# Kernel optimization log

Measured on AMD Instinct MI355X. Metric: run time of the kernel, lower is better.

Reference implementation:

```python
import jax, jax.numpy as jnp
import numpy as np


def setup_inputs() -> dict:
    key = jax.random.key(0)
    k1, = jax.random.split(key, 1)
    x = jax.random.normal(k1, (8, 256, 128, 128), dtype=jnp.float32)
    alpha = jnp.ones((1,), dtype=jnp.float32)
    return {"x": x, "alpha": alpha}


def reference(x, alpha):
    B, C, H, W = x.shape
    v = x.reshape(B, C, H * W)                 # [B, C, HW] (query=key=value)
    energy = jnp.einsum('bcs,bds->bcd', v, v)  # [B, C, C]
    # max-softmax: softmax(max(energy) - energy) along last dim
    energy_new = jnp.max(energy, axis=-1, keepdims=True) - energy
    w = jax.nn.softmax(energy_new, axis=-1)    # [B, C, C]
    y = jnp.einsum('bcd,bds->bcs', w, v)       # [B, C, HW]
    y = y.reshape(B, C, H, W)
    return alpha * y + x
```

## Files before the change

### kernel.cpp

```cpp
#include <hip/hip_runtime.h>
#include <math.h>

static constexpr int Bn = 8;
static constexpr int Cn = 256;
static constexpr int Sn = 16384;

typedef __bf16 bf16x4 __attribute__((ext_vector_type(4)));
typedef __bf16 bf16x8 __attribute__((ext_vector_type(8)));
typedef float  f32x4  __attribute__((ext_vector_type(4)));

__device__ __forceinline__ void split_store(__bf16* __restrict__ Hi, __bf16* __restrict__ Lo,
                                            int row, int kq, float4 v) {
  __bf16 h0 = (__bf16)v.x, h1 = (__bf16)v.y, h2 = (__bf16)v.z, h3 = (__bf16)v.w;
  int off = row * 32 + (((kq >> 1) ^ (row & 3)) << 3) + ((kq & 1) << 2);
  *(bf16x4*)&Hi[off] = (bf16x4){h0, h1, h2, h3};
  *(bf16x4*)&Lo[off] = (bf16x4){(__bf16)(v.x - (float)h0), (__bf16)(v.y - (float)h1),
                                (__bf16)(v.z - (float)h2), (__bf16)(v.w - (float)h3)};
}

__device__ __forceinline__ bf16x8 frag_ld(const __bf16* __restrict__ P, int row, int quad) {
  return *(const bf16x8*)&P[row * 32 + ((quad ^ (row & 3)) << 3)];
}

static constexpr int TILE   = 128;
static constexpr int KSPLIT = 16;
static constexpr int KSLICE = Sn / KSPLIT;
static constexpr int KB     = 32;

__global__ __launch_bounds__(256, 2) void gram_kernel(const float* __restrict__ x,
                                                      float* __restrict__ energy) {
  const int b    = blockIdx.z;
  const int tsel = blockIdx.y;
  const int kk   = blockIdx.x;
  const int ti   = (tsel == 1) ? 1 : 0;
  const int tj   = (tsel == 0) ? 0 : 1;
  const bool diag = (tsel < 2);

  const float* vb    = x + (size_t)b * Cn * Sn;
  const float* Abase = vb + (size_t)(ti * TILE) * Sn + kk * KSLICE;
  const float* Bbase = vb + (size_t)(tj * TILE) * Sn + kk * KSLICE;

  __shared__ __align__(16) __bf16 Ah[TILE * 32];
  __shared__ __align__(16) __bf16 Al[TILE * 32];
  __shared__ __align__(16) __bf16 Bh[TILE * 32];
  __shared__ __align__(16) __bf16 Bl[TILE * 32];

  const int t    = threadIdx.x;
  const int lane = t & 63;
  const int wv   = t >> 6;
  const int wr   = wv >> 1;
  const int wc   = wv & 1;
  const int ln   = lane & 15;
  const int quad = lane >> 4;

  const int srow = t >> 3;
  const int skq  = t & 7;

  float4 areg[4], breg[4];

#pragma unroll
  for (int it = 0; it < 4; it++)
    areg[it] = *(const float4*)(Abase + (size_t)(srow + it * 32) * Sn + skq * 4);
  if (!diag) {
#pragma unroll
    for (int it = 0; it < 4; it++)
      breg[it] = *(const float4*)(Bbase + (size_t)(srow + it * 32) * Sn + skq * 4);
  }

  f32x4 acc[4][4];
#pragma unroll
  for (int i = 0; i < 4; i++)
#pragma unroll
    for (int j = 0; j < 4; j++) acc[i][j] = (f32x4){0.f, 0.f, 0.f, 0.f};

  for (int kc = 0; kc < KSLICE; kc += KB) {
#pragma unroll
    for (int it = 0; it < 4; it++) split_store(Ah, Al, srow + it * 32, skq, areg[it]);
    if (!diag) {
#pragma unroll
      for (int it = 0; it < 4; it++) split_store(Bh, Bl, srow + it * 32, skq, breg[it]);
    }
    __syncthreads();

    const __bf16* PH = diag ? Ah : Bh;
    const __bf16* PL = diag ? Al : Bl;

    bf16x8 fah[4], fal[4];
#pragma unroll
    for (int i = 0; i < 4; i++) {
      int ar = wr * 64 + i * 16 + ln;
      fah[i] = frag_ld(Ah, ar, quad);
      fal[i] = frag_ld(Al, ar, quad);
    }

    if (kc + KB < KSLICE) {
#pragma unroll
      for (int it = 0; it < 4; it++)
        areg[it] = *(const float4*)(Abase + (size_t)(srow + it * 32) * Sn + (kc + KB) + skq * 4);
      if (!diag) {
#pragma unroll
        for (int it = 0; it < 4; it++)
          breg[it] = *(const float4*)(Bbase + (size_t)(srow + it * 32) * Sn + (kc + KB) + skq * 4);
      }
    }

#pragma unroll
    for (int j = 0; j < 4; j++) {
      int br = wc * 64 + j * 16 + ln;
      bf16x8 fbh = frag_ld(PH, br, quad);
      bf16x8 fbl = frag_ld(PL, br, quad);
#pragma unroll
      for (int i = 0; i < 4; i++) {
        acc[i][j] = __builtin_amdgcn_mfma_f32_16x16x32_bf16(fah[i], fbh, acc[i][j], 0, 0, 0);
        acc[i][j] = __builtin_amdgcn_mfma_f32_16x16x32_bf16(fah[i], fbl, acc[i][j], 0, 0, 0);
        acc[i][j] = __builtin_amdgcn_mfma_f32_16x16x32_bf16(fal[i], fbh, acc[i][j], 0, 0, 0);
      }
    }
    __syncthreads();
  }

  float* E = energy + (size_t)b * Cn * Cn;
#pragma unroll
  for (int i = 0; i < 4; i++)
#pragma unroll
    for (int j = 0; j < 4; j++) {
      int c0 = ti * TILE + wr * 64 + i * 16 + quad * 4;
      int d  = tj * TILE + wc * 64 + j * 16 + ln;
#pragma unroll
      for (int r = 0; r < 4; r++) {
        float v = acc[i][j][r];
        atomicAdd(&E[(size_t)(c0 + r) * Cn + d], v);
        if (tsel == 2) atomicAdd(&E[(size_t)d * Cn + (c0 + r)], v);
      }
    }
}

__global__ __launch_bounds__(256) void softmax_kernel(float* __restrict__ energy) {
  const int wv   = threadIdx.x >> 6;
  const int lane = threadIdx.x & 63;
  const int row  = blockIdx.x * 4 + wv;

  float4 e = *(const float4*)&energy[(size_t)row * Cn + lane * 4];
  float m = fminf(fminf(e.x, e.y), fminf(e.z, e.w));
#pragma unroll
  for (int off = 32; off > 0; off >>= 1) m = fminf(m, __shfl_xor(m, off));

  float4 p;
  p.x = expf(m - e.x); p.y = expf(m - e.y);
  p.z = expf(m - e.z); p.w = expf(m - e.w);
  float s = p.x + p.y + p.z + p.w;
#pragma unroll
  for (int off = 32; off > 0; off >>= 1) s += __shfl_xor(s, off);

  float inv = 1.f / s;
  p.x *= inv; p.y *= inv; p.z *= inv; p.w *= inv;
  *(float4*)&energy[(size_t)row * Cn + lane * 4] = p;
}

__global__ __launch_bounds__(256, 2) void ygemm_mfma_kernel(const float* __restrict__ w,
                                                            const float* __restrict__ x,
                                                            const float* __restrict__ alpha,
                                                            float* __restrict__ out) {
  const int b  = blockIdx.z;
  const int m0 = blockIdx.y * 128;
  const int s0 = blockIdx.x * 128;

  const float* Wb = w + ((size_t)b * Cn + m0) * Cn;
  const float* Vb = x + (size_t)b * Cn * Sn;

  __shared__ __align__(16) __bf16 Ah[128 * 32];
  __shared__ __align__(16) __bf16 Al[128 * 32];
  __shared__ __align__(16) __bf16 Bh[128 * 32];
  __shared__ __align__(16) __bf16 Bl[128 * 32];

  const int t    = threadIdx.x;
  const int lane = t & 63;
  const int wv   = t >> 6;
  const int wr   = wv >> 1;
  const int wc   = wv & 1;
  const int ln   = lane & 15;
  const int quad = lane >> 4;

  const int srow = t >> 3;
  const int skq  = t & 7;

  float4 areg[4];
  float  breg[16];

#pragma unroll
  for (int it = 0; it < 4; it++)
    areg[it] = *(const float4*)(Wb + (size_t)(srow + it * 32) * Cn + skq * 4);
#pragma unroll
  for (int it = 0; it < 4; it++) {
    const float* col = Vb + (size_t)(skq * 4) * Sn + s0 + srow + it * 32;
    breg[it * 4 + 0] = col[0];
    breg[it * 4 + 1] = col[(size_t)Sn];
    breg[it * 4 + 2] = col[(size_t)2 * Sn];
    breg[it * 4 + 3] = col[(size_t)3 * Sn];
  }

  f32x4 acc[4][4];
#pragma unroll
  for (int i = 0; i < 4; i++)
#pragma unroll
    for (int j = 0; j < 4; j++) acc[i][j] = (f32x4){0.f, 0.f, 0.f, 0.f};

  for (int kc = 0; kc < Cn; kc += KB) {
#pragma unroll
    for (int it = 0; it < 4; it++) split_store(Ah, Al, srow + it * 32, skq, areg[it]);
#pragma unroll
    for (int it = 0; it < 4; it++) {
      float4 bv = make_float4(breg[it * 4 + 0], breg[it * 4 + 1],
                              breg[it * 4 + 2], breg[it * 4 + 3]);
      split_store(Bh, Bl, srow + it * 32, skq, bv);
    }
    __syncthreads();

    bf16x8 fah[4], fal[4];
#pragma unroll
    for (int i = 0; i < 4; i++) {
      int ar = wr * 64 + i * 16 + ln;
      fah[i] = frag_ld(Ah, ar, quad);
      fal[i] = frag_ld(Al, ar, quad);
    }

    if (kc + KB < Cn) {
#pragma unroll
      for (int it = 0; it < 4; it++)
        areg[it] = *(const float4*)(Wb + (size_t)(srow + it * 32) * Cn + (kc + KB) + skq * 4);
#pragma unroll
      for (int it = 0; it < 4; it++) {
        const float* col = Vb + (size_t)((kc + KB) + skq * 4) * Sn + s0 + srow + it * 32;
        breg[it * 4 + 0] = col[0];
        breg[it * 4 + 1] = col[(size_t)Sn];
        breg[it * 4 + 2] = col[(size_t)2 * Sn];
        breg[it * 4 + 3] = col[(size_t)3 * Sn];
      }
    }

#pragma unroll
    for (int j = 0; j < 4; j++) {
      int br = wc * 64 + j * 16 + ln;
      bf16x8 fbh = frag_ld(Bh, br, quad);
      bf16x8 fbl = frag_ld(Bl, br, quad);
#pragma unroll
      for (int i = 0; i < 4; i++) {
        acc[i][j] = __builtin_amdgcn_mfma_f32_16x16x32_bf16(fah[i], fbh, acc[i][j], 0, 0, 0);
        acc[i][j] = __builtin_amdgcn_mfma_f32_16x16x32_bf16(fah[i], fbl, acc[i][j], 0, 0, 0);
        acc[i][j] = __builtin_amdgcn_mfma_f32_16x16x32_bf16(fal[i], fbh, acc[i][j], 0, 0, 0);
      }
    }
    __syncthreads();
  }

  const float al = alpha[0];
#pragma unroll
  for (int i = 0; i < 4; i++)
#pragma unroll
    for (int j = 0; j < 4; j++) {
      int c = m0 + wr * 64 + i * 16 + quad * 4;
      int s = s0 + wc * 64 + j * 16 + ln;
      const float* xr = x   + ((size_t)b * Cn + c) * Sn + s;
      float*       op = out + ((size_t)b * Cn + c) * Sn + s;
#pragma unroll
      for (int r = 0; r < 4; r++)
        op[(size_t)r * Sn] = al * acc[i][j][r] + xr[(size_t)r * Sn];
    }
}

extern "C" void kernel_launch(void* const* d_in, const int* in_sizes, int n_in,
                              void* d_out, int out_size, void* d_ws, size_t ws_size,
                              hipStream_t stream) {
  const float* x     = (const float*)d_in[0];
  const float* alpha = (const float*)d_in[1];
  float*       out   = (float*)d_out;
  float*       energy = (float*)d_ws;

  const size_t energy_bytes = (size_t)Bn * Cn * Cn * sizeof(float);
  hipMemsetAsync(energy, 0, energy_bytes, stream);

  dim3 g1(KSPLIT, 3, Bn);
  gram_kernel<<<g1, 256, 0, stream>>>(x, energy);

  softmax_kernel<<<(Bn * Cn) / 4, 256, 0, stream>>>(energy);

  dim3 g3(Sn / 128, Cn / 128, Bn);
  ygemm_mfma_kernel<<<g3, 256, 0, stream>>>(energy, x, alpha, out);
}
```

Before: 350.7 us.

## Fuse memset, Gram, softmax and output GEMM into one persistent kernel

Replaces the memset plus three kernel launches with a single persistent kernel whose grid is sized to occupancy and capped at 512 blocks. The stages (zeroing energy, split-K Gram with atomics, row softmax, output GEMM with residual) are separated by software grid barriers built on global atomic counters. The Gram split is also changed: diagonal tiles use 32 K-slices and the off-diagonal tile uses 64. This aims to remove launch gaps and inter-kernel tails, at the cost of grid-barrier spinning, fewer blocks available to hide latency in the memory-bound GEMM, and a deadlock risk if not all blocks are co-resident.

Measured after the change: 543.8 us. 1.55x slower.

```diff
diff --git a/kernel.cpp b/kernel.cpp
--- a/kernel.cpp
+++ b/kernel.cpp
@@ -8,6 +8,9 @@
 typedef __bf16 bf16x4 __attribute__((ext_vector_type(4)));
 typedef __bf16 bf16x8 __attribute__((ext_vector_type(8)));
 typedef float  f32x4  __attribute__((ext_vector_type(4)));
+
+static constexpr int TILE = 128;
+static constexpr int KB   = 32;
 
 __device__ __forceinline__ void split_store(__bf16* __restrict__ Hi, __bf16* __restrict__ Lo,
                                             int row, int kq, float4 v) {
@@ -22,10 +25,263 @@
   return *(const bf16x8*)&P[row * 32 + ((quad ^ (row & 3)) << 3)];
 }
 
-static constexpr int TILE   = 128;
+__device__ unsigned g_cnt[4] = {0, 0, 0, 0};
+__device__ unsigned g_gen[4] = {0, 0, 0, 0};
+
+__device__ __forceinline__ void grid_barrier(int slot) {
+  __syncthreads();
+  if (threadIdx.x == 0) {
+    __threadfence();
+    unsigned my = __hip_atomic_load(&g_gen[slot], __ATOMIC_RELAXED, __HIP_MEMORY_SCOPE_AGENT);
+    unsigned n  = gridDim.x;
+    unsigned a  = __hip_atomic_fetch_add(&g_cnt[slot], 1u, __ATOMIC_ACQ_REL,
+                                         __HIP_MEMORY_SCOPE_AGENT) + 1u;
+    if (a == n) {
+      __hip_atomic_store(&g_cnt[slot], 0u, __ATOMIC_RELAXED, __HIP_MEMORY_SCOPE_AGENT);
+      __hip_atomic_fetch_add(&g_gen[slot], 1u, __ATOMIC_RELEASE, __HIP_MEMORY_SCOPE_AGENT);
+    } else {
+      while (__hip_atomic_load(&g_gen[slot], __ATOMIC_RELAXED, __HIP_MEMORY_SCOPE_AGENT) == my)
+        __builtin_amdgcn_s_sleep(2);
+    }
+    __threadfence();
+  }
+  __syncthreads();
+}
+
+__global__ __launch_bounds__(256, 2) void fused_kernel(const float* __restrict__ x,
+                                                       const float* __restrict__ alpha,
+                                                       float* __restrict__ out,
+                                                       float* __restrict__ energy) {
+  __shared__ __align__(16) __bf16 Ah[TILE * 32];
+  __shared__ __align__(16) __bf16 Al[TILE * 32];
+  __shared__ __align__(16) __bf16 Bh[TILE * 32];
+  __shared__ __align__(16) __bf16 Bl[TILE * 32];
+
+  const int t    = threadIdx.x;
+  const int lane = t & 63;
+  const int wv   = t >> 6;
+  const int wr   = wv >> 1;
+  const int wc   = wv & 1;
+  const int ln   = lane & 15;
+  const int quad = lane >> 4;
+  const int srow = t >> 3;
+  const int skq  = t & 7;
+
+  {
+    const int total = (Bn * Cn * Cn) / 4;
+    for (int i = blockIdx.x * 256 + t; i < total; i += gridDim.x * 256)
+      *(float4*)&energy[(size_t)i * 4] = (float4){0.f, 0.f, 0.f, 0.f};
+  }
+  grid_barrier(0);
+
+  for (unsigned job = blockIdx.x; job < 1024; job += gridDim.x) {
+    int b, ti, tj, kk, ksl;
+    bool diag;
+    if (job < 512) {
+      b = job >> 6; int r = job & 63;
+      diag = true; ti = tj = (r >> 5); kk = r & 31; ksl = 512;
+    } else {
+      unsigned j2 = job - 512;
+      b = j2 >> 6; kk = j2 & 63;
+      diag = false; ti = 0; tj = 1; ksl = 256;
+    }
+
+    const float* vb    = x + (size_t)b * Cn * Sn;
+    const float* Abase = vb + (size_t)(ti * TILE) * Sn + (size_t)kk * ksl;
+    const float* Bbase = vb + (size_t)(tj * TILE) * Sn + (size_t)kk * ksl;
+
+    float4 areg[4], breg[4];
+#pragma unroll
+    for (int it = 0; it < 4; it++)
+      areg[it] = *(const float4*)(Abase + (size_t)(srow + it * 32) * Sn + skq * 4);
+    if (!diag) {
+#pragma unroll
+      for (int it = 0; it < 4; it++)
+        breg[it] = *(const float4*)(Bbase + (size_t)(srow + it * 32) * Sn + skq * 4);
+    }
+
+    f32x4 acc[4][4];
+#pragma unroll
+    for (int i = 0; i < 4; i++)
+#pragma unroll
+      for (int j = 0; j < 4; j++) acc[i][j] = (f32x4){0.f, 0.f, 0.f, 0.f};
+
+    for (int kc = 0; kc < ksl; kc += KB) {
+#pragma unroll
+      for (int it = 0; it < 4; it++) split_store(Ah, Al, srow + it * 32, skq, areg[it]);
+      if (!diag) {
+#pragma unroll
+        for (int it = 0; it < 4; it++) split_store(Bh, Bl, srow + it * 32, skq, breg[it]);
+      }
+      __syncthreads();
+
+      const __bf16* PH = diag ? Ah : Bh;
+      const __bf16* PL = diag ? Al : Bl;
+
+      bf16x8 fah[4], fal[4];
+#pragma unroll
+      for (int i = 0; i < 4; i++) {
+        int ar = wr * 64 + i * 16 + ln;
+        fah[i] = frag_ld(Ah, ar, quad);
+        fal[i] = frag_ld(Al, ar, quad);
+      }
+
+      if (kc + KB < ksl) {
+#pragma unroll
+        for (int it = 0; it < 4; it++)
+          areg[it] = *(const float4*)(Abase + (size_t)(srow + it * 32) * Sn + (kc + KB) + skq * 4);
+        if (!diag) {
+#pragma unroll
+          for (int it = 0; it < 4; it++)
+            breg[it] = *(const float4*)(Bbase + (size_t)(srow + it * 32) * Sn + (kc + KB) + skq * 4);
+        }
+      }
+
+#pragma unroll
+      for (int j = 0; j < 4; j++) {
+        int br = wc * 64 + j * 16 + ln;
+        bf16x8 fbh = frag_ld(PH, br, quad);
+        bf16x8 fbl = frag_ld(PL, br, quad);
+#pragma unroll
+        for (int i = 0; i < 4; i++) {
+          acc[i][j] = __builtin_amdgcn_mfma_f32_16x16x32_bf16(fah[i], fbh, acc[i][j], 0, 0, 0);
+          acc[i][j] = __builtin_amdgcn_mfma_f32_16x16x32_bf16(fah[i], fbl, acc[i][j], 0, 0, 0);
+          acc[i][j] = __builtin_amdgcn_mfma_f32_16x16x32_bf16(fal[i], fbh, acc[i][j], 0, 0, 0);
+        }
+      }
+      __syncthreads();
+    }
+
+    float* E = energy + (size_t)b * Cn * Cn;
+#pragma unroll
+    for (int i = 0; i < 4; i++)
+#pragma unroll
+      for (int j = 0; j < 4; j++) {
+        int c0 = ti * TILE + wr * 64 + i * 16 + quad * 4;
+        int d  = tj * TILE + wc * 64 + j * 16 + ln;
+#pragma unroll
+        for (int r = 0; r < 4; r++) {
+          float v = acc[i][j][r];
+          atomicAdd(&E[(size_t)(c0 + r) * Cn + d], v);
+          if (!diag) atomicAdd(&E[(size_t)d * Cn + (c0 + r)], v);
+        }
+      }
+  }
+  grid_barrier(1);
+
+  for (int row = blockIdx.x * 4 + wv; row < Bn * Cn; row += gridDim.x * 4) {
+    float4 e = *(const float4*)&energy[(size_t)row * Cn + lane * 4];
+    float m = fminf(fminf(e.x, e.y), fminf(e.z, e.w));
+#pragma unroll
+    for (int off = 32; off > 0; off >>= 1) m = fminf(m, __shfl_xor(m, off));
+    float4 p;
+    p.x = expf(m - e.x); p.y = expf(m - e.y);
+    p.z = expf(m - e.z); p.w = expf(m - e.w);
+    float s = p.x + p.y + p.z + p.w;
+#pragma unroll
+    for (int off = 32; off > 0; off >>= 1) s += __shfl_xor(s, off);
+    float inv = 1.f / s;
+    p.x *= inv; p.y *= inv; p.z *= inv; p.w *= inv;
+    *(float4*)&energy[(size_t)row * Cn + lane * 4] = p;
+  }
+  grid_barrier(2);
+
+  const float al = alpha[0];
+  for (unsigned jj = blockIdx.x; jj < 2048; jj += gridDim.x) {
+    const int b  = jj >> 8;
+    const int m0 = ((jj >> 7) & 1) * 128;
+    const int s0 = (jj & 127) * 128;
+
+    const float* Wb = energy + ((size_t)b * Cn + m0) * Cn;
+    const float* Vb = x + (size_t)b * Cn * Sn;
+
+    float4 areg[4];
+    float  breg[16];
+#pragma unroll
+    for (int it = 0; it < 4; it++)
+      areg[it] = *(const float4*)(Wb + (size_t)(srow + it * 32) * Cn + skq * 4);
+#pragma unroll
+    for (int it = 0; it < 4; it++) {
+      const float* col = Vb + (size_t)(skq * 4) * Sn + s0 + srow + it * 32;
+      breg[it * 4 + 0] = col[0];
+      breg[it * 4 + 1] = col[(size_t)Sn];
+      breg[it * 4 + 2] = col[(size_t)2 * Sn];
+      breg[it * 4 + 3] = col[(size_t)3 * Sn];
+    }
+
+    f32x4 acc[4][4];
+#pragma unroll
+    for (int i = 0; i < 4; i++)
+#pragma unroll
+      for (int j = 0; j < 4; j++) acc[i][j] = (f32x4){0.f, 0.f, 0.f, 0.f};
+
+    for (int kc = 0; kc < Cn; kc += KB) {
+#pragma unroll
+      for (int it = 0; it < 4; it++) split_store(Ah, Al, srow + it * 32, skq, areg[it]);
+#pragma unroll
+      for (int it = 0; it < 4; it++) {
+        float4 bv = make_float4(breg[it * 4 + 0], breg[it * 4 + 1],
+                                breg[it * 4 + 2], breg[it * 4 + 3]);
+        split_store(Bh, Bl, srow + it * 32, skq, bv);
+      }
+      __syncthreads();
+
+      bf16x8 fah[4], fal[4];
+#pragma unroll
+      for (int i = 0; i < 4; i++) {
+        int ar = wr * 64 + i * 16 + ln;
+        fah[i] = frag_ld(Ah, ar, quad);
+        fal[i] = frag_ld(Al, ar, quad);
+      }
+
+      if (kc + KB < Cn) {
+#pragma unroll
+        for (int it = 0; it < 4; it++)
+          areg[it] = *(const float4*)(Wb + (size_t)(srow + it * 32) * Cn + (kc + KB) + skq * 4);
+#pragma unroll
+        for (int it = 0; it < 4; it++) {
+          const float* col = Vb + (size_t)((kc + KB) + skq * 4) * Sn + s0 + srow + it * 32;
+          breg[it * 4 + 0] = col[0];
+          breg[it * 4 + 1] = col[(size_t)Sn];
+          breg[it * 4 + 2] = col[(size_t)2 * Sn];
+          breg[it * 4 + 3] = col[(size_t)3 * Sn];
+        }
+      }
+
+#pragma unroll
+      for (int j = 0; j < 4; j++) {
+        int br = wc * 64 + j * 16 + ln;
+        bf16x8 fbh = frag_ld(Bh, br, quad);
+        bf16x8 fbl = frag_ld(Bl, br, quad);
+#pragma unroll
+        for (int i = 0; i < 4; i++) {
+          acc[i][j] = __builtin_amdgcn_mfma_f32_16x16x32_bf16(fah[i], fbh, acc[i][j], 0, 0, 0);
+          acc[i][j] = __builtin_amdgcn_mfma_f32_16x16x32_bf16(fah[i], fbl, acc[i][j], 0, 0, 0);
+          acc[i][j] = __builtin_amdgcn_mfma_f32_16x16x32_bf16(fal[i], fbh, acc[i][j], 0, 0, 0);
+        }
+      }
+      __syncthreads();
+    }
+
+    const float* xb = x   + (size_t)b * Cn * Sn;
+    float*       ob = out + (size_t)b * Cn * Sn;
+#pragma unroll
+    for (int i = 0; i < 4; i++)
+#pragma unroll
+      for (int j = 0; j < 4; j++) {
+        int c = m0 + wr * 64 + i * 16 + quad * 4;
+        int s = s0 + wc * 64 + j * 16 + ln;
+        const float* xr = xb + (size_t)c * Sn + s;
+        float*       op = ob + (size_t)c * Sn + s;
+#pragma unroll
+        for (int r = 0; r < 4; r++)
+          op[(size_t)r * Sn] = al * acc[i][j][r] + xr[(size_t)r * Sn];
+      }
+  }
+}
+
 static constexpr int KSPLIT = 16;
 static constexpr int KSLICE = Sn / KSPLIT;
-static constexpr int KB     = 32;
 
 __global__ __launch_bounds__(256, 2) void gram_kernel(const float* __restrict__ x,
                                                       float* __restrict__ energy) {
@@ -52,12 +308,10 @@
   const int wc   = wv & 1;
   const int ln   = lane & 15;
   const int quad = lane >> 4;
-
   const int srow = t >> 3;
   const int skq  = t & 7;
 
   float4 areg[4], breg[4];
-
 #pragma unroll
   for (int it = 0; it < 4; it++)
     areg[it] = *(const float4*)(Abase + (size_t)(srow + it * 32) * Sn + skq * 4);
@@ -180,7 +434,6 @@
   const int wc   = wv & 1;
   const int ln   = lane & 15;
   const int quad = lane >> 4;
-
   const int srow = t >> 3;
   const int skq  = t & 7;
 
@@ -276,14 +529,30 @@
   float*       out   = (float*)d_out;
   float*       energy = (float*)d_ws;
 
-  const size_t energy_bytes = (size_t)Bn * Cn * Cn * sizeof(float);
-  hipMemsetAsync(energy, 0, energy_bytes, stream);
-
-  dim3 g1(KSPLIT, 3, Bn);
-  gram_kernel<<<g1, 256, 0, stream>>>(x, energy);
-
-  softmax_kernel<<<(Bn * Cn) / 4, 256, 0, stream>>>(energy);
-
-  dim3 g3(Sn / 128, Cn / 128, Bn);
-  ygemm_mfma_kernel<<<g3, 256, 0, stream>>>(energy, x, alpha, out);
-}
+  static int g_grid = -2;
+  if (g_grid == -2) {
+    int nb = 0, cu = 0;
+    hipDeviceProp_t prop;
+    if (hipGetDeviceProperties(&prop, 0) == hipSuccess) cu = prop.multiProcessorCount;
+    if (cu > 0 &&
+        hipOccupancyMaxActiveBlocksPerMultiprocessor(&nb, fused_kernel, 256, 0) == hipSuccess &&
+        nb >= 1) {
+      long g = (long)nb * cu;
+      g_grid = (int)(g > 512 ? 512 : g);
+    } else {
+      g_grid = 0;
+    }
+  }
+
+  if (g_grid >= 64) {
+    fused_kernel<<<dim3(g_grid), dim3(256), 0, stream>>>(x, alpha, out, energy);
+  } else {
+    const size_t energy_bytes = (size_t)Bn * Cn * Cn * sizeof(float);
+    hipMemsetAsync(energy, 0, energy_bytes, stream);
+    dim3 g1(KSPLIT, 3, Bn);
+    gram_kernel<<<g1, 256, 0, stream>>>(x, energy);
+    softmax_kernel<<<(Bn * Cn) / 4, 256, 0, stream>>>(energy);
+    dim3 g3(Sn / 128, Cn / 128, Bn);
+    ygemm_mfma_kernel<<<g3, 256, 0, stream>>>(energy, x, alpha, out);
+  }
+}
```

## Double-buffer LDS in both GEMMs and rebalance gram work split

Applied to the files above, without the earlier changes.

Both MFMA GEMM kernels now use two LDS buffers, so the next K-chunk is split and stored while the current chunk feeds the MFMAs. This removes one barrier per iteration and lets global loads run two chunks ahead. The gram kernel also moves to a flat 1024-block grid in which diagonal tiles get half-length K slices and the off-diagonal tile, which loads twice the data, gets quarter-length slices, to even out per-block work. The cost is doubled LDS use (64KB per block), which may lower occupancy, plus more atomic adds into the energy buffer.

Result: slower. 459.9 us (+31.1%).

```diff
diff --git a/kernel.cpp b/kernel.cpp
--- a/kernel.cpp
+++ b/kernel.cpp
@@ -8,6 +8,9 @@
 typedef __bf16 bf16x4 __attribute__((ext_vector_type(4)));
 typedef __bf16 bf16x8 __attribute__((ext_vector_type(8)));
 typedef float  f32x4  __attribute__((ext_vector_type(4)));
+
+static constexpr int TILE = 128;
+static constexpr int KB   = 32;
 
 __device__ __forceinline__ void split_store(__bf16* __restrict__ Hi, __bf16* __restrict__ Lo,
                                             int row, int kq, float4 v) {
@@ -22,28 +25,27 @@
   return *(const bf16x8*)&P[row * 32 + ((quad ^ (row & 3)) << 3)];
 }
 
-static constexpr int TILE   = 128;
-static constexpr int KSPLIT = 16;
-static constexpr int KSLICE = Sn / KSPLIT;
-static constexpr int KB     = 32;
-
 __global__ __launch_bounds__(256, 2) void gram_kernel(const float* __restrict__ x,
                                                       float* __restrict__ energy) {
-  const int b    = blockIdx.z;
-  const int tsel = blockIdx.y;
-  const int kk   = blockIdx.x;
-  const int ti   = (tsel == 1) ? 1 : 0;
-  const int tj   = (tsel == 0) ? 0 : 1;
-  const bool diag = (tsel < 2);
+  const int job  = blockIdx.x;
+  const bool diag = (job < 512);
+  int b, ti, tj, kk, ksl;
+  if (diag) {
+    b = job >> 6; int r = job & 63;
+    ti = tj = r >> 5; kk = r & 31; ksl = 512;
+  } else {
+    int j2 = job - 512;
+    b = j2 >> 6; kk = j2 & 63; ti = 0; tj = 1; ksl = 256;
+  }
 
   const float* vb    = x + (size_t)b * Cn * Sn;
-  const float* Abase = vb + (size_t)(ti * TILE) * Sn + kk * KSLICE;
-  const float* Bbase = vb + (size_t)(tj * TILE) * Sn + kk * KSLICE;
-
-  __shared__ __align__(16) __bf16 Ah[TILE * 32];
-  __shared__ __align__(16) __bf16 Al[TILE * 32];
-  __shared__ __align__(16) __bf16 Bh[TILE * 32];
-  __shared__ __align__(16) __bf16 Bl[TILE * 32];
+  const float* Abase = vb + (size_t)(ti * TILE) * Sn + (size_t)kk * ksl;
+  const float* Bbase = vb + (size_t)(tj * TILE) * Sn + (size_t)kk * ksl;
+
+  __shared__ __align__(16) __bf16 Ah[2][TILE * 32];
+  __shared__ __align__(16) __bf16 Al[2][TILE * 32];
+  __shared__ __align__(16) __bf16 Bh[2][TILE * 32];
+  __shared__ __align__(16) __bf16 Bl[2][TILE * 32];
 
   const int t    = threadIdx.x;
   const int lane = t & 63;
@@ -52,7 +54,6 @@
   const int wc   = wv & 1;
   const int ln   = lane & 15;
   const int quad = lane >> 4;
-
   const int srow = t >> 3;
   const int skq  = t & 7;
 
@@ -66,6 +67,21 @@
     for (int it = 0; it < 4; it++)
       breg[it] = *(const float4*)(Bbase + (size_t)(srow + it * 32) * Sn + skq * 4);
   }
+#pragma unroll
+  for (int it = 0; it < 4; it++) split_store(Ah[0], Al[0], srow + it * 32, skq, areg[it]);
+  if (!diag) {
+#pragma unroll
+    for (int it = 0; it < 4; it++) split_store(Bh[0], Bl[0], srow + it * 32, skq, breg[it]);
+  }
+#pragma unroll
+  for (int it = 0; it < 4; it++)
+    areg[it] = *(const float4*)(Abase + (size_t)(srow + it * 32) * Sn + KB + skq * 4);
+  if (!diag) {
+#pragma unroll
+    for (int it = 0; it < 4; it++)
+      breg[it] = *(const float4*)(Bbase + (size_t)(srow + it * 32) * Sn + KB + skq * 4);
+  }
+  __syncthreads();
 
   f32x4 acc[4][4];
 #pragma unroll
@@ -73,42 +89,45 @@
 #pragma unroll
     for (int j = 0; j < 4; j++) acc[i][j] = (f32x4){0.f, 0.f, 0.f, 0.f};
 
-  for (int kc = 0; kc < KSLICE; kc += KB) {
-#pragma unroll
-    for (int it = 0; it < 4; it++) split_store(Ah, Al, srow + it * 32, skq, areg[it]);
-    if (!diag) {
-#pragma unroll
-      for (int it = 0; it < 4; it++) split_store(Bh, Bl, srow + it * 32, skq, breg[it]);
-    }
-    __syncthreads();
-
-    const __bf16* PH = diag ? Ah : Bh;
-    const __bf16* PL = diag ? Al : Bl;
+  int p = 0;
+  for (int kc = 0; kc < ksl; kc += KB, p ^= 1) {
+    const __bf16* pAh = Ah[p];
+    const __bf16* pAl = Al[p];
+    const __bf16* pBh = diag ? Ah[p] : Bh[p];
+    const __bf16* pBl = diag ? Al[p] : Bl[p];
 
     bf16x8 fah[4], fal[4];
 #pragma unroll
     for (int i = 0; i < 4; i++) {
       int ar = wr * 64 + i * 16 + ln;
-      fah[i] = frag_ld(Ah, ar, quad);
-      fal[i] = frag_ld(Al, ar, quad);
-    }
-
-    if (kc + KB < KSLICE) {
+      fah[i] = frag_ld(pAh, ar, quad);
+      fal[i] = frag_ld(pAl, ar, quad);
+    }
+
+    if (kc + KB < ksl) {
+#pragma unroll
+      for (int it = 0; it < 4; it++) split_store(Ah[p ^ 1], Al[p ^ 1], srow + it * 32, skq, areg[it]);
+      if (!diag) {
+#pragma unroll
+        for (int it = 0; it < 4; it++) split_store(Bh[p ^ 1], Bl[p ^ 1], srow + it * 32, skq, breg[it]);
+      }
+    }
+    if (kc + 2 * KB < ksl) {
 #pragma unroll
       for (int it = 0; it < 4; it++)
-        areg[it] = *(const float4*)(Abase + (size_t)(srow + it * 32) * Sn + (kc + KB) + skq * 4);
+        areg[it] = *(const float4*)(Abase + (size_t)(srow + it * 32) * Sn + (kc + 2 * KB) + skq * 4);
       if (!diag) {
 #pragma unroll
         for (int it = 0; it < 4; it++)
-          breg[it] = *(const float4*)(Bbase + (size_t)(srow + it * 32) * Sn + (kc + KB) + skq * 4);
+          breg[it] = *(const float4*)(Bbase + (size_t)(srow + it * 32) * Sn + (kc + 2 * KB) + skq * 4);
       }
     }
 
 #pragma unroll
     for (int j = 0; j < 4; j++) {
       int br = wc * 64 + j * 16 + ln;
-      bf16x8 fbh = frag_ld(PH, br, quad);
-      bf16x8 fbl = frag_ld(PL, br, quad);
+      bf16x8 fbh = frag_ld(pBh, br, quad);
+      bf16x8 fbl = frag_ld(pBl, br, quad);
 #pragma unroll
       for (int i = 0; i < 4; i++) {
         acc[i][j] = __builtin_amdgcn_mfma_f32_16x16x32_bf16(fah[i], fbh, acc[i][j], 0, 0, 0);
@@ -130,7 +149,7 @@
       for (int r = 0; r < 4; r++) {
         float v = acc[i][j][r];
         atomicAdd(&E[(size_t)(c0 + r) * Cn + d], v);
-        if (tsel == 2) atomicAdd(&E[(size_t)d * Cn + (c0 + r)], v);
+        if (!diag) atomicAdd(&E[(size_t)d * Cn + (c0 + r)], v);
       }
     }
 }
@@ -168,10 +187,10 @@
   const float* Wb = w + ((size_t)b * Cn + m0) * Cn;
   const float* Vb = x + (size_t)b * Cn * Sn;
 
-  __shared__ __align__(16) __bf16 Ah[128 * 32];
-  __shared__ __align__(16) __bf16 Al[128 * 32];
-  __shared__ __align__(16) __bf16 Bh[128 * 32];
-  __shared__ __align__(16) __bf16 Bl[128 * 32];
+  __shared__ __align__(16) __bf16 Ah[2][128 * 32];
+  __shared__ __align__(16) __bf16 Al[2][128 * 32];
+  __shared__ __align__(16) __bf16 Bh[2][128 * 32];
+  __shared__ __align__(16) __bf16 Bl[2][128 * 32];
 
   const int t    = threadIdx.x;
   const int lane = t & 63;
@@ -180,7 +199,6 @@
   const int wc   = wv & 1;
   const int ln   = lane & 15;
   const int quad = lane >> 4;
-
   const int srow = t >> 3;
   const int skq  = t & 7;
 
@@ -198,6 +216,26 @@
     breg[it * 4 + 2] = col[(size_t)2 * Sn];
     breg[it * 4 + 3] = col[(size_t)3 * Sn];
   }
+#pragma unroll
+  for (int it = 0; it < 4; it++) split_store(Ah[0], Al[0], srow + it * 32, skq, areg[it]);
+#pragma unroll
+  for (int it = 0; it < 4; it++) {
+    float4 bv = make_float4(breg[it * 4 + 0], breg[it * 4 + 1],
+                            breg[it * 4 + 2], breg[it * 4 + 3]);
+    split_store(Bh[0], Bl[0], srow + it * 32, skq, bv);
+  }
+#pragma unroll
+  for (int it = 0; it < 4; it++)
+    areg[it] = *(const float4*)(Wb + (size_t)(srow + it * 32) * Cn + KB + skq * 4);
+#pragma unroll
+  for (int it = 0; it < 4; it++) {
+    const float* col = Vb + (size_t)(KB + skq * 4) * Sn + s0 + srow + it * 32;
+    breg[it * 4 + 0] = col[0];
+    breg[it * 4 + 1] = col[(size_t)Sn];
+    breg[it * 4 + 2] = col[(size_t)2 * Sn];
+    breg[it * 4 + 3] = col[(size_t)3 * Sn];
+  }
+  __syncthreads();
 
   f32x4 acc[4][4];
 #pragma unroll
@@ -205,32 +243,33 @@
 #pragma unroll
     for (int j = 0; j < 4; j++) acc[i][j] = (f32x4){0.f, 0.f, 0.f, 0.f};
 
-  for (int kc = 0; kc < Cn; kc += KB) {
-#pragma unroll
-    for (int it = 0; it < 4; it++) split_store(Ah, Al, srow + it * 32, skq, areg[it]);
-#pragma unroll
-    for (int it = 0; it < 4; it++) {
-      float4 bv = make_float4(breg[it * 4 + 0], breg[it * 4 + 1],
-                              breg[it * 4 + 2], breg[it * 4 + 3]);
-      split_store(Bh, Bl, srow + it * 32, skq, bv);
-    }
-    __syncthreads();
-
+  int p = 0;
+  for (int kc = 0; kc < Cn; kc += KB, p ^= 1) {
     bf16x8 fah[4], fal[4];
 #pragma unroll
     for (int i = 0; i < 4; i++) {
       int ar = wr * 64 + i * 16 + ln;
-      fah[i] = frag_ld(Ah, ar, quad);
-      fal[i] = frag_ld(Al, ar, quad);
+      fah[i] = frag_ld(Ah[p], ar, quad);
+      fal[i] = frag_ld(Al[p], ar, quad);
     }
 
     if (kc + KB < Cn) {
 #pragma unroll
+      for (int it = 0; it < 4; it++) split_store(Ah[p ^ 1], Al[p ^ 1], srow + it * 32, skq, areg[it]);
+#pragma unroll
+      for (int it = 0; it < 4; it++) {
+        float4 bv = make_float4(breg[it * 4 + 0], breg[it * 4 + 1],
+                                breg[it * 4 + 2], breg[it * 4 + 3]);
+        split_store(Bh[p ^ 1], Bl[p ^ 1], srow + it * 32, skq, bv);
+      }
+    }
+    if (kc + 2 * KB < Cn) {
+#pragma unroll
       for (int it = 0; it < 4; it++)
-        areg[it] = *(const float4*)(Wb + (size_t)(srow + it * 32) * Cn + (kc + KB) + skq * 4);
+        areg[it] = *(const float4*)(Wb + (size_t)(srow + it * 32) * Cn + (kc + 2 * KB) + skq * 4);
 #pragma unroll
       for (int it = 0; it < 4; it++) {
-        const float* col = Vb + (size_t)((kc + KB) + skq * 4) * Sn + s0 + srow + it * 32;
+        const float* col = Vb + (size_t)((kc + 2 * KB) + skq * 4) * Sn + s0 + srow + it * 32;
         breg[it * 4 + 0] = col[0];
         breg[it * 4 + 1] = col[(size_t)Sn];
         breg[it * 4 + 2] = col[(size_t)2 * Sn];
@@ -241,8 +280,8 @@
 #pragma unroll
     for (int j = 0; j < 4; j++) {
       int br = wc * 64 + j * 16 + ln;
-      bf16x8 fbh = frag_ld(Bh, br, quad);
-      bf16x8 fbl = frag_ld(Bl, br, quad);
+      bf16x8 fbh = frag_ld(Bh[p], br, quad);
+      bf16x8 fbl = frag_ld(Bl[p], br, quad);
 #pragma unroll
       for (int i = 0; i < 4; i++) {
         acc[i][j] = __builtin_amdgcn_mfma_f32_16x16x32_bf16(fah[i], fbh, acc[i][j], 0, 0, 0);
@@ -279,8 +318,7 @@
   const size_t energy_bytes = (size_t)Bn * Cn * Cn * sizeof(float);
   hipMemsetAsync(energy, 0, energy_bytes, stream);
 
-  dim3 g1(KSPLIT, 3, Bn);
-  gram_kernel<<<g1, 256, 0, stream>>>(x, energy);
+  gram_kernel<<<dim3(1024), 256, 0, stream>>>(x, energy);
 
   softmax_kernel<<<(Bn * Cn) / 4, 256, 0, stream>>>(energy);
 
```
